# Performance work log

Measured on AMD Instinct MI355X. Metric: run time of the kernel, lower is better.

## Reference

```python
import jax, jax.numpy as jnp
import numpy as np

N = 50000      # nodes
E = 800000     # edges (avg degree 16)
H = 128        # hidden_dim
GDIM = 64      # global feature dim
G = 10         # DiffGroupNorm groups
LAMDA = 0.01
EPS = 1e-5


def setup_inputs() -> dict:
    key = jax.random.key(0)
    ks = jax.random.split(key, 24)
    s = 0.05
    inp = {
        "x": jax.random.normal(ks[0], (N, H), dtype=jnp.float32),
        "edge_index": jax.random.randint(ks[1], (2, E), 0, N, dtype=jnp.int32),
        "edge_features": jax.random.normal(ks[2], (E, H), dtype=jnp.float32),
        "global_feat": jax.random.normal(ks[3], (1, GDIM), dtype=jnp.float32),
        # combine: Dense(H) on concat [x | messages | global] -> (H+H+GDIM, H)
        "Wc": jax.random.normal(ks[4], (H + H + GDIM, H), dtype=jnp.float32) * s,
        "bc": jnp.zeros((H,), jnp.float32),
    }
    for i, tag in enumerate(["a", "b"]):
        k = jax.random.split(ks[5 + i], 4)
        inp[f"W1{tag}"] = jax.random.normal(k[0], (H, H), dtype=jnp.float32) * s
        inp[f"b1{tag}"] = jnp.zeros((H,), jnp.float32)
        inp[f"W2{tag}"] = jax.random.normal(k[1], (H, H), dtype=jnp.float32) * s
        inp[f"b2{tag}"] = jnp.zeros((H,), jnp.float32)
        inp[f"linW{tag}"] = jax.random.normal(k[2], (H, G), dtype=jnp.float32) * s
        inp[f"linb{tag}"] = jnp.zeros((G,), jnp.float32)
        inp[f"gamma{tag}"] = jnp.ones((G * H,), jnp.float32)
        inp[f"beta{tag}"] = jnp.zeros((G * H,), jnp.float32)
    return inp


def _diff_group_norm(x, linW, linb, gamma, beta):
    # DiffGroupNorm: soft group assignment + per-(group,channel) batch norm.
    n, f = x.shape
    s = jax.nn.softmax(x @ linW + linb, axis=-1)            # [N, G]
    o = (s[:, :, None] * x[:, None, :]).reshape(n, G * f)   # [N, G*F]
    mu = o.mean(axis=0)
    var = o.var(axis=0)
    o = (o - mu) * jax.lax.rsqrt(var + EPS) * gamma + beta
    return x + LAMDA * o.reshape(n, G, f).sum(axis=1)


def _block(out, W1, b1, W2, b2, linW, linb, gamma, beta):
    h = jax.nn.softplus(out @ W1 + b1) @ W2 + b2
    h = _diff_group_norm(h, linW, linb, gamma, beta)
    return out + h


def reference(x, edge_index, edge_features, global_feat, Wc, bc,
              W1a, b1a, W2a, b2a, linWa, linba, gammaa, betaa,
              W1b, b1b, W2b, b2b, linWb, linbb, gammab, betab):
    n = x.shape[0]
    row = edge_index[0]
    # tf.scatter_nd accumulates duplicates -> segment sum over destination nodes
    messages = jax.ops.segment_sum(edge_features, row, num_segments=n)
    g = jnp.repeat(global_feat, n // global_feat.shape[0], axis=0)
    combined = jnp.concatenate([x, messages, g], axis=-1)
    out = jax.nn.softplus(combined @ Wc + bc)
    initial = out
    out = _block(out, W1a, b1a, W2a, b2a, linWa, linba, gammaa, betaa)
    out = _block(out, W1b, b1b, W2b, b2b, linWb, linbb, gammab, betab)
    return out + initial
```

## Files before the change

kernel.cpp:

```cpp
#include <hip/hip_runtime.h>
#include <math.h>

constexpr int NN = 50000;
constexpr int NE = 800000;
constexpr int HD = 128;
constexpr int NG = 10;
constexpr float LAM = 0.01f;
constexpr float EPSV = 1e-5f;
constexpr int NBLK = (NN + 255) / 256;

typedef __attribute__((ext_vector_type(8))) short s8v;
typedef __attribute__((ext_vector_type(4))) float f4v;

__device__ __forceinline__ float softplus_f(float x) {
    return fmaxf(x, 0.f) + log1pf(expf(-fabsf(x)));
}
__device__ __forceinline__ unsigned short f2b(float f) {
    unsigned u = __float_as_uint(f);
    unsigned r = (u + 0x7FFFu + ((u >> 16) & 1u)) >> 16;
    return (unsigned short)r;
}
__device__ __forceinline__ float b2f(unsigned short u) {
    return __uint_as_float(((unsigned)u) << 16);
}

__global__ __launch_bounds__(256) void hist_kernel(
    const int* __restrict__ rows, int* __restrict__ cnt)
{
    int e = blockIdx.x * 256 + threadIdx.x;
    if (e < NE) atomicAdd(&cnt[rows[e]], 1);
}

__global__ __launch_bounds__(256) void scan1_kernel(
    const int* __restrict__ cnt, int* __restrict__ bsum)
{
    __shared__ int red[256];
    int t = threadIdx.x;
    int i = blockIdx.x * 256 + t;
    red[t] = (i < NN) ? cnt[i] : 0;
    __syncthreads();
    for (int d = 128; d > 0; d >>= 1) {
        if (t < d) red[t] += red[t + d];
        __syncthreads();
    }
    if (t == 0) bsum[blockIdx.x] = red[0];
}

__global__ __launch_bounds__(256) void scan2_kernel(
    const int* __restrict__ bsum, int* __restrict__ bbase)
{
    __shared__ int sh[256];
    int t = threadIdx.x;
    int v = (t < NBLK) ? bsum[t] : 0;
    sh[t] = v;
    __syncthreads();
    for (int d = 1; d < 256; d <<= 1) {
        int u = (t >= d) ? sh[t - d] : 0;
        __syncthreads();
        sh[t] += u;
        __syncthreads();
    }
    if (t < NBLK) bbase[t] = sh[t] - v;
}

__global__ __launch_bounds__(256) void scan3_kernel(
    const int* __restrict__ cnt, const int* __restrict__ bbase,
    int* __restrict__ off, int* __restrict__ cur)
{
    __shared__ int sh[256];
    int t = threadIdx.x;
    int i = blockIdx.x * 256 + t;
    int v = (i < NN) ? cnt[i] : 0;
    sh[t] = v;
    __syncthreads();
    for (int d = 1; d < 256; d <<= 1) {
        int u = (t >= d) ? sh[t - d] : 0;
        __syncthreads();
        sh[t] += u;
        __syncthreads();
    }
    int excl = sh[t] - v + bbase[blockIdx.x];
    if (i < NN) { off[i] = excl; cur[i] = excl; }
    if (i == NN - 1) off[NN] = NE;
}

__global__ __launch_bounds__(256) void fill_kernel(
    const int* __restrict__ rows, int* __restrict__ cur, int* __restrict__ eid)
{
    int e = blockIdx.x * 256 + threadIdx.x;
    if (e < NE) {
        int slot = atomicAdd(&cur[rows[e]], 1);
        eid[slot] = e;
    }
}

__global__ __launch_bounds__(256) void gather_kernel(
    const float* __restrict__ ef, const int* __restrict__ off,
    const int* __restrict__ eid, uint2* __restrict__ msgbf)
{
    int node = blockIdx.x * 4 + (threadIdx.x >> 6);
    if (node >= NN) return;
    int lane = threadIdx.x & 63;
    int half = lane >> 5, lc = lane & 31;
    int b = off[node], e = off[node + 1];
    float4 acc = make_float4(0.f, 0.f, 0.f, 0.f);
    for (int i = b + half; i < e; i += 2) {
        int ed = eid[i];
        float4 v = *reinterpret_cast<const float4*>(ef + (size_t)ed * HD + lc * 4);
        acc.x += v.x; acc.y += v.y; acc.z += v.z; acc.w += v.w;
    }
    acc.x += __shfl_xor(acc.x, 32);
    acc.y += __shfl_xor(acc.y, 32);
    acc.z += __shfl_xor(acc.z, 32);
    acc.w += __shfl_xor(acc.w, 32);
    if (half == 0) {
        uint2 pk;
        pk.x = (unsigned)f2b(acc.x) | ((unsigned)f2b(acc.y) << 16);
        pk.y = (unsigned)f2b(acc.z) | ((unsigned)f2b(acc.w) << 16);
        msgbf[(size_t)node * 32 + lc] = pk;
    }
}

__global__ __launch_bounds__(256) void prep_kernel(
    const float* __restrict__ Wc,
    const float* __restrict__ W1a, const float* __restrict__ W2a,
    const float* __restrict__ W1b, const float* __restrict__ W2b,
    short* __restrict__ wct, short* __restrict__ wts)
{
    int i = blockIdx.x * 256 + threadIdx.x;
    if (i < 40960) {
        int n = i / 320, kk = i % 320;
        wct[i] = (short)f2b(Wc[kk * 128 + n]);
    } else if (i < 40960 + 4 * 16384) {
        int j = i - 40960;
        int mat = j >> 14;
        int idx = j & 16383;
        int n = idx >> 7, kk = idx & 127;
        const float* src = (mat == 0) ? W1a : (mat == 1) ? W2a : (mat == 2) ? W1b : W2b;
        wts[j] = (short)f2b(src[kk * 128 + n]);
    }
}

__global__ __launch_bounds__(256) void combine_mfma_kernel(
    const float* __restrict__ x, const short* __restrict__ msgbf,
    const float* __restrict__ gf, const short* __restrict__ wct,
    const float* __restrict__ bc,
    unsigned short* __restrict__ outbf, unsigned short* __restrict__ initbf)
{
    __shared__ short As[64 * 72];
    __shared__ short Ws[128 * 72];
    __shared__ float bcs[128];
    const int tid = threadIdx.x;
    const int m0 = blockIdx.x * 64;
    if (tid < 128) bcs[tid] = bc[tid];
    const int lane = tid & 63;
    const int wv = tid >> 6;
    const int fr = lane & 15;
    const int fc = lane >> 4;

    f4v acc[8];
    #pragma unroll
    for (int ct = 0; ct < 8; ++ct) acc[ct] = (f4v){0.f, 0.f, 0.f, 0.f};

    const int arow = tid >> 2;
    const int aseg = (tid & 3) * 16;
    const int wcol = tid >> 1;
    const int wseg = (tid & 1) * 32;

    for (int c = 0; c < 5; ++c) {
        const int k0 = c * 64;
        {
            short tmp[16];
            int grow = m0 + arow;
            if (grow >= NN) {
                #pragma unroll
                for (int j = 0; j < 16; ++j) tmp[j] = 0;
            } else if (c < 2) {
                const float* src = x + (size_t)grow * 128 + k0 + aseg;
                #pragma unroll
                for (int q = 0; q < 4; ++q) {
                    float4 v = *reinterpret_cast<const float4*>(src + 4 * q);
                    tmp[4*q+0] = (short)f2b(v.x); tmp[4*q+1] = (short)f2b(v.y);
                    tmp[4*q+2] = (short)f2b(v.z); tmp[4*q+3] = (short)f2b(v.w);
                }
            } else if (c < 4) {
                const short* src = msgbf + (size_t)grow * 128 + (k0 - 128) + aseg;
                *(s8v*)tmp = *(const s8v*)src;
                *(s8v*)(tmp + 8) = *(const s8v*)(src + 8);
            } else {
                const float* src = gf + aseg;
                #pragma unroll
                for (int q = 0; q < 4; ++q) {
                    float4 v = *reinterpret_cast<const float4*>(src + 4 * q);
                    tmp[4*q+0] = (short)f2b(v.x); tmp[4*q+1] = (short)f2b(v.y);
                    tmp[4*q+2] = (short)f2b(v.z); tmp[4*q+3] = (short)f2b(v.w);
                }
            }
            *(s8v*)&As[arow * 72 + aseg] = *(s8v*)tmp;
            *(s8v*)&As[arow * 72 + aseg + 8] = *(s8v*)(tmp + 8);
        }
        {
            const short* src = wct + (size_t)wcol * 320 + k0 + wseg;
            #pragma unroll
            for (int j = 0; j < 4; ++j)
                *(s8v*)&Ws[wcol * 72 + wseg + 8 * j] = *(const s8v*)(src + 8 * j);
        }
        __syncthreads();
        const short* ap = As + (wv * 16 + fr) * 72 + fc * 8;
        const short* bp = Ws + fr * 72 + fc * 8;
        #pragma unroll
        for (int ks = 0; ks < 2; ++ks) {
            s8v a = *(const s8v*)(ap + ks * 32);
            #pragma unroll
            for (int ct = 0; ct < 8; ++ct) {
                s8v b = *(const s8v*)(bp + ct * 16 * 72 + ks * 32);
                acc[ct] = __builtin_amdgcn_mfma_f32_16x16x32_bf16(a, b, acc[ct], 0, 0, 0);
            }
        }
        __syncthreads();
    }
    const int rbase = m0 + wv * 16 + fc * 4;
    #pragma unroll
    for (int ct = 0; ct < 8; ++ct) {
        int col = ct * 16 + fr;
        float bv = bcs[col];
        #pragma unroll
        for (int r = 0; r < 4; ++r) {
            int row = rbase + r;
            if (row < NN) {
                unsigned short b = f2b(softplus_f(acc[ct][r] + bv));
                outbf[(size_t)row * 128 + col] = b;
                initbf[(size_t)row * 128 + col] = b;
            }
        }
    }
}

__global__ __launch_bounds__(256) void fused12_kernel(
    const unsigned short* __restrict__ outbf, const short* __restrict__ w1t,
    const short* __restrict__ w2t, const float* __restrict__ b1,
    const float* __restrict__ b2, const float* __restrict__ linW,
    const float* __restrict__ linb,
    unsigned short* __restrict__ hbf, float* __restrict__ sout)
{
    __shared__ short As[64 * 136];
    __shared__ short Ws[128 * 136];
    __shared__ short Ts[64 * 136];
    __shared__ float b1s[128], b2s[128];
    __shared__ float lws[128 * 11];
    __shared__ float lbs[10];
    const int tid = threadIdx.x;
    const int m0 = blockIdx.x * 64;
    if (tid < 128) { b1s[tid] = b1[tid]; b2s[tid] = b2[tid]; }
    for (int i = tid; i < 1280; i += 256) lws[(i / 10) * 11 + (i % 10)] = linW[i];
    if (tid < 10) lbs[tid] = linb[tid];
    const int lane = tid & 63;
    const int wv = tid >> 6;
    const int fr = lane & 15;
    const int fc = lane >> 4;

    {
        int row = tid >> 2, seg = (tid & 3) * 32;
        int grow = m0 + row;
        s8v v[4];
        if (grow < NN) {
            const short* src = (const short*)outbf + (size_t)grow * 128 + seg;
            #pragma unroll
            for (int j = 0; j < 4; ++j) v[j] = *(const s8v*)(src + 8 * j);
        } else {
            s8v z = {0,0,0,0,0,0,0,0};
            #pragma unroll
            for (int j = 0; j < 4; ++j) v[j] = z;
        }
        #pragma unroll
        for (int j = 0; j < 4; ++j) *(s8v*)&As[row * 136 + seg + 8 * j] = v[j];
    }
    {
        int col = tid >> 1, seg = (tid & 1) * 64;
        const short* src = w1t + (size_t)col * 128 + seg;
        #pragma unroll
        for (int j = 0; j < 8; ++j)
            *(s8v*)&Ws[col * 136 + seg + 8 * j] = *(const s8v*)(src + 8 * j);
    }
    __syncthreads();

    f4v acc[8];
    #pragma unroll
    for (int ct = 0; ct < 8; ++ct) acc[ct] = (f4v){0.f, 0.f, 0.f, 0.f};
    {
        const short* ap = As + (wv * 16 + fr) * 136 + fc * 8;
        const short* bp = Ws + fr * 136 + fc * 8;
        #pragma unroll
        for (int ks = 0; ks < 4; ++ks) {
            s8v a = *(const s8v*)(ap + ks * 32);
            #pragma unroll
            for (int ct = 0; ct < 8; ++ct) {
                s8v b = *(const s8v*)(bp + ct * 16 * 136 + ks * 32);
                acc[ct] = __builtin_amdgcn_mfma_f32_16x16x32_bf16(a, b, acc[ct], 0, 0, 0);
            }
        }
    }
    {
        int rb = wv * 16 + fc * 4;
        #pragma unroll
        for (int ct = 0; ct < 8; ++ct) {
            int col = ct * 16 + fr;
            float bv = b1s[col];
            #pragma unroll
            for (int r = 0; r < 4; ++r)
                Ts[(rb + r) * 136 + col] = (short)f2b(softplus_f(acc[ct][r] + bv));
        }
    }
    __syncthreads();
    {
        int col = tid >> 1, seg = (tid & 1) * 64;
        const short* src = w2t + (size_t)col * 128 + seg;
        #pragma unroll
        for (int j = 0; j < 8; ++j)
            *(s8v*)&Ws[col * 136 + seg + 8 * j] = *(const s8v*)(src + 8 * j);
    }
    __syncthreads();

    #pragma unroll
    for (int ct = 0; ct < 8; ++ct) acc[ct] = (f4v){0.f, 0.f, 0.f, 0.f};
    {
        const short* ap = Ts + (wv * 16 + fr) * 136 + fc * 8;
        const short* bp = Ws + fr * 136 + fc * 8;
        #pragma unroll
        for (int ks = 0; ks < 4; ++ks) {
            s8v a = *(const s8v*)(ap + ks * 32);
            #pragma unroll
            for (int ct = 0; ct < 8; ++ct) {
                s8v b = *(const s8v*)(bp + ct * 16 * 136 + ks * 32);
                acc[ct] = __builtin_amdgcn_mfma_f32_16x16x32_bf16(a, b, acc[ct], 0, 0, 0);
            }
        }
    }
    #pragma unroll
    for (int ct = 0; ct < 8; ++ct) {
        float bv = b2s[ct * 16 + fr];
        #pragma unroll
        for (int r = 0; r < 4; ++r) acc[ct][r] += bv;
    }
    float dot[4][10];
    #pragma unroll
    for (int r = 0; r < 4; ++r)
        #pragma unroll
        for (int g = 0; g < 10; ++g) dot[r][g] = 0.f;
    #pragma unroll
    for (int ct = 0; ct < 8; ++ct) {
        #pragma unroll
        for (int g = 0; g < 10; ++g) {
            float lwv = lws[(ct * 16 + fr) * 11 + g];
            #pragma unroll
            for (int r = 0; r < 4; ++r) dot[r][g] += acc[ct][r] * lwv;
        }
    }
    #pragma unroll
    for (int r = 0; r < 4; ++r)
        #pragma unroll
        for (int g = 0; g < 10; ++g) {
            float v = dot[r][g];
            v += __shfl_xor(v, 1);
            v += __shfl_xor(v, 2);
            v += __shfl_xor(v, 4);
            v += __shfl_xor(v, 8);
            dot[r][g] = v + lbs[g];
        }
    #pragma unroll
    for (int r = 0; r < 4; ++r) {
        float m = dot[r][0];
        #pragma unroll
        for (int g = 1; g < 10; ++g) m = fmaxf(m, dot[r][g]);
        float sum = 0.f;
        #pragma unroll
        for (int g = 0; g < 10; ++g) { dot[r][g] = expf(dot[r][g] - m); sum += dot[r][g]; }
        float inv = 1.f / sum;
        #pragma unroll
        for (int g = 0; g < 10; ++g) dot[r][g] *= inv;
    }
    const int growb = m0 + wv * 16 + fc * 4;
    #pragma unroll
    for (int ct = 0; ct < 8; ++ct) {
        int col = ct * 16 + fr;
        #pragma unroll
        for (int r = 0; r < 4; ++r) {
            int row = growb + r;
            if (row < NN) hbf[(size_t)row * 128 + col] = f2b(acc[ct][r]);
        }
    }
    if (fr < 10) {
        #pragma unroll
        for (int r = 0; r < 4; ++r) {
            int row = growb + r;
            if (row < NN) {
                float v = 0.f;
                #pragma unroll
                for (int g = 0; g < 10; ++g) v = (fr == g) ? dot[r][g] : v;
                sout[(size_t)row * 10 + fr] = v;
            }
        }
    }
}

__global__ __launch_bounds__(256) void stats_kernel(
    const unsigned short* __restrict__ hbf, const float* __restrict__ s,
    float* __restrict__ sum1, float* __restrict__ sum2)
{
    __shared__ float hs[64 * 128];
    __shared__ float ss[640];
    const int tid = threadIdx.x;
    const int c = tid & 127;
    const int g0 = (tid >> 7) * 5;
    float a1[5], a2[5];
    #pragma unroll
    for (int q = 0; q < 5; ++q) { a1[q] = 0.f; a2[q] = 0.f; }

    const int nchunks = (NN + 63) / 64;
    for (int chunk = blockIdx.x; chunk < nchunks; chunk += gridDim.x) {
        int nbase = chunk * 64;
        #pragma unroll
        for (int i = 0; i < 4; ++i) {
            int f = tid + i * 256;
            int row = f >> 4, col = (f & 15) * 8;
            int n = nbase + row;
            if (n < NN) {
                s8v raw = *(const s8v*)((const short*)hbf + (size_t)n * 128 + col);
                #pragma unroll
                for (int j = 0; j < 8; ++j)
                    hs[row * 128 + col + j] = b2f((unsigned short)raw[j]);
            } else {
                #pragma unroll
                for (int j = 0; j < 8; ++j) hs[row * 128 + col + j] = 0.f;
            }
        }
        for (int idx = tid; idx < 640; idx += 256) {
            int n = nbase + idx / 10;
            ss[idx] = (n < NN) ? s[(size_t)n * 10 + idx % 10] : 0.f;
        }
        __syncthreads();
        int nmax = min(64, NN - nbase);
        for (int n = 0; n < nmax; ++n) {
            float hv = hs[n * 128 + c];
            #pragma unroll
            for (int q = 0; q < 5; ++q) {
                float p = ss[n * 10 + g0 + q] * hv;
                a1[q] += p;
                a2[q] += p * p;
            }
        }
        __syncthreads();
    }
    #pragma unroll
    for (int q = 0; q < 5; ++q) {
        atomicAdd(&sum1[(g0 + q) * 128 + c], a1[q]);
        atomicAdd(&sum2[(g0 + q) * 128 + c], a2[q]);
    }
}

__global__ void finalize_kernel(
    const float* __restrict__ sum1, const float* __restrict__ sum2,
    const float* __restrict__ gamma, const float* __restrict__ beta,
    float* __restrict__ w, float* __restrict__ kvec)
{
    int c = threadIdx.x;
    float kacc = 0.f;
    const float invn = 1.f / (float)NN;
    for (int g = 0; g < NG; ++g) {
        int idx = g * 128 + c;
        float mu = sum1[idx] * invn;
        float var = sum2[idx] * invn - mu * mu;
        float inv = rsqrtf(var + EPSV);
        float wg = inv * gamma[idx];
        w[idx] = wg;
        kacc += beta[idx] - mu * wg;
    }
    kvec[c] = kacc;
}

template<bool LAST>
__global__ __launch_bounds__(256) void apply_kernel(
    const unsigned short* __restrict__ outbf_in,
    const unsigned short* __restrict__ hbf,
    const float* __restrict__ s, const float* __restrict__ w,
    const float* __restrict__ kvec, const unsigned short* __restrict__ initbf,
    float* __restrict__ dstf, unsigned short* __restrict__ outbf_out)
{
    __shared__ __align__(16) float ws_[1280];
    __shared__ float ks_[128];
    __shared__ float ss_[640];
    const int tid = threadIdx.x;
    const int m0 = blockIdx.x * 64;
    for (int i = tid; i < 320; i += 256)
        ((float4*)ws_)[i] = ((const float4*)w)[i];
    if (tid < 128) ks_[tid] = kvec[tid];
    for (int i = tid; i < 640; i += 256) {
        int n = m0 + i / 10;
        ss_[i] = (n < NN) ? s[(size_t)n * 10 + i % 10] : 0.f;
    }
    __syncthreads();
    const int tc = tid & 31, rg = tid >> 5;
    #pragma unroll
    for (int p = 0; p < 8; ++p) {
        int nl = p * 8 + rg;
        int n = m0 + nl;
        if (n >= NN) continue;
        float A0 = 0.f, A1 = 0.f, A2 = 0.f, A3 = 0.f;
        #pragma unroll
        for (int g = 0; g < 10; ++g) {
            float sv = ss_[nl * 10 + g];
            float4 wv = *reinterpret_cast<const float4*>(&ws_[g * 128 + tc * 4]);
            A0 += sv * wv.x; A1 += sv * wv.y; A2 += sv * wv.z; A3 += sv * wv.w;
        }
        ushort4 hv4 = *reinterpret_cast<const ushort4*>(hbf + (size_t)n * 128 + tc * 4);
        ushort4 ov4 = *reinterpret_cast<const ushort4*>(outbf_in + (size_t)n * 128 + tc * 4);
        float h0 = b2f(hv4.x), h1 = b2f(hv4.y), h2 = b2f(hv4.z), h3 = b2f(hv4.w);
        float r0 = b2f(ov4.x) + h0 + LAM * (h0 * A0 + ks_[tc * 4 + 0]);
        float r1 = b2f(ov4.y) + h1 + LAM * (h1 * A1 + ks_[tc * 4 + 1]);
        float r2 = b2f(ov4.z) + h2 + LAM * (h2 * A2 + ks_[tc * 4 + 2]);
        float r3 = b2f(ov4.w) + h3 + LAM * (h3 * A3 + ks_[tc * 4 + 3]);
        if (LAST) {
            ushort4 iv4 = *reinterpret_cast<const ushort4*>(initbf + (size_t)n * 128 + tc * 4);
            r0 += b2f(iv4.x); r1 += b2f(iv4.y); r2 += b2f(iv4.z); r3 += b2f(iv4.w);
            float4 o = make_float4(r0, r1, r2, r3);
            *reinterpret_cast<float4*>(dstf + (size_t)n * 128 + tc * 4) = o;
        } else {
            ushort4 o;
            o.x = f2b(r0); o.y = f2b(r1); o.z = f2b(r2); o.w = f2b(r3);
            *reinterpret_cast<ushort4*>(outbf_out + (size_t)n * 128 + tc * 4) = o;
        }
    }
}

extern "C" void kernel_launch(void* const* d_in, const int* in_sizes, int n_in,
                              void* d_out, int out_size, void* d_ws, size_t ws_size,
                              hipStream_t stream)
{
    const float* x    = (const float*)d_in[0];
    const int*   eidx = (const int*)  d_in[1];
    const float* ef   = (const float*)d_in[2];
    const float* gf   = (const float*)d_in[3];
    const float* Wc   = (const float*)d_in[4];
    const float* bc   = (const float*)d_in[5];

    float* p = (float*)d_ws;
    int*   cnt  = (int*)p;
    float* sums = p + NN;
    p += NN + 4 * 1280;
    unsigned short* msgbf  = (unsigned short*)p;  p += (size_t)NN * 64;
    unsigned short* outbf  = (unsigned short*)p;  p += (size_t)NN * 64;
    unsigned short* initbf = (unsigned short*)p;  p += (size_t)NN * 64;
    unsigned short* hbf    = (unsigned short*)p;  p += (size_t)NN * 64;
    float* sbuf = p;                              p += (size_t)NN * 10;
    float* wbuf = p;                              p += 1280;
    float* kvec = p;                              p += 128;
    short* wct  = (short*)p;
    short* wts  = wct + 40960;

    int* off   = (int*)initbf;
    int* cur   = off + NN + 1;
    int* bsum  = cur + NN;
    int* bbase = bsum + NBLK;
    int* eid   = (int*)hbf;

    prep_kernel<<<416, 256, 0, stream>>>(
        Wc, (const float*)d_in[6], (const float*)d_in[8],
        (const float*)d_in[14], (const float*)d_in[16], wct, wts);

    hipMemsetAsync(cnt, 0, sizeof(int) * (NN + 4 * 1280), stream);

    hist_kernel <<<(NE + 255) / 256, 256, 0, stream>>>(eidx, cnt);
    scan1_kernel<<<NBLK, 256, 0, stream>>>(cnt, bsum);
    scan2_kernel<<<1, 256, 0, stream>>>(bsum, bbase);
    scan3_kernel<<<NBLK, 256, 0, stream>>>(cnt, bbase, off, cur);
    fill_kernel <<<(NE + 255) / 256, 256, 0, stream>>>(eidx, cur, eid);
    gather_kernel<<<(NN + 3) / 4, 256, 0, stream>>>(ef, off, eid, (uint2*)msgbf);

    const int gblocks = (NN + 63) / 64;
    combine_mfma_kernel<<<gblocks, 256, 0, stream>>>(
        x, (const short*)msgbf, gf, wct, bc, outbf, initbf);

    for (int b = 0; b < 2; ++b) {
        const float* b1    = (const float*)d_in[7 + 8 * b];
        const float* b2    = (const float*)d_in[9 + 8 * b];
        const float* linW  = (const float*)d_in[10 + 8 * b];
        const float* linb  = (const float*)d_in[11 + 8 * b];
        const float* gamma = (const float*)d_in[12 + 8 * b];
        const float* beta  = (const float*)d_in[13 + 8 * b];
        const short* w1t = wts + (size_t)(2 * b) * 16384;
        const short* w2t = wts + (size_t)(2 * b + 1) * 16384;
        float* sum1 = sums + (size_t)b * 2560;
        float* sum2 = sum1 + 1280;

        fused12_kernel<<<gblocks, 256, 0, stream>>>(
            outbf, w1t, w2t, b1, b2, linW, linb, hbf, sbuf);
        stats_kernel<<<256, 256, 0, stream>>>(hbf, sbuf, sum1, sum2);
        finalize_kernel<<<1, 128, 0, stream>>>(sum1, sum2, gamma, beta, wbuf, kvec);
        if (b == 0)
            apply_kernel<false><<<gblocks, 256, 0, stream>>>(
                outbf, hbf, sbuf, wbuf, kvec, nullptr, nullptr, outbf);
        else
            apply_kernel<true><<<gblocks, 256, 0, stream>>>(
                outbf, hbf, sbuf, wbuf, kvec, initbf, (float*)d_out, nullptr);
    }
}
```

Before: 436.2 us.

## Fuse group-norm stats into GEMM kernel and drop duplicate init buffer

Per-block DiffGroupNorm partial sums are now computed inside fused12_kernel from the tile still held in LDS and written to a per-block buffer. A small deterministic reduce kernel replaces the stats kernel with global atomics, and finalize is folded into apply_kernel. The two-pass prefix scan is merged into one kernel, hist and fill are vectorised to four edges per thread, and ping-pong output buffers remove the duplicate init write. This cuts the re-read of h, the atomics and several launches, at the cost of more LDS in fused12, which may lower occupancy.

```diff
diff --git a/kernel.cpp b/kernel.cpp
--- a/kernel.cpp
+++ b/kernel.cpp
@@ -8,6 +8,7 @@
 constexpr float LAM = 0.01f;
 constexpr float EPSV = 1e-5f;
 constexpr int NBLK = (NN + 255) / 256;
+constexpr int GBLK = (NN + 63) / 64;
 
 typedef __attribute__((ext_vector_type(8))) short s8v;
 typedef __attribute__((ext_vector_type(4))) float f4v;
@@ -27,8 +28,14 @@
 __global__ __launch_bounds__(256) void hist_kernel(
     const int* __restrict__ rows, int* __restrict__ cnt)
 {
-    int e = blockIdx.x * 256 + threadIdx.x;
-    if (e < NE) atomicAdd(&cnt[rows[e]], 1);
+    int base = (blockIdx.x * 256 + threadIdx.x) * 4;
+    if (base < NE) {
+        int4 r = *reinterpret_cast<const int4*>(rows + base);
+        atomicAdd(&cnt[r.x], 1);
+        atomicAdd(&cnt[r.y], 1);
+        atomicAdd(&cnt[r.z], 1);
+        atomicAdd(&cnt[r.w], 1);
+    }
 }
 
 __global__ __launch_bounds__(256) void scan1_kernel(
@@ -46,40 +53,29 @@
     if (t == 0) bsum[blockIdx.x] = red[0];
 }
 
-__global__ __launch_bounds__(256) void scan2_kernel(
-    const int* __restrict__ bsum, int* __restrict__ bbase)
+__global__ __launch_bounds__(256) void scan3_kernel(
+    const int* __restrict__ cnt, const int* __restrict__ bsum,
+    int* __restrict__ off, int* __restrict__ cur)
 {
     __shared__ int sh[256];
-    int t = threadIdx.x;
-    int v = (t < NBLK) ? bsum[t] : 0;
-    sh[t] = v;
-    __syncthreads();
-    for (int d = 1; d < 256; d <<= 1) {
-        int u = (t >= d) ? sh[t - d] : 0;
-        __syncthreads();
-        sh[t] += u;
-        __syncthreads();
-    }
-    if (t < NBLK) bbase[t] = sh[t] - v;
-}
-
-__global__ __launch_bounds__(256) void scan3_kernel(
-    const int* __restrict__ cnt, const int* __restrict__ bbase,
-    int* __restrict__ off, int* __restrict__ cur)
-{
-    __shared__ int sh[256];
+    __shared__ int bs[256];
+    __shared__ int basev;
     int t = threadIdx.x;
     int i = blockIdx.x * 256 + t;
-    int v = (i < NN) ? cnt[i] : 0;
-    sh[t] = v;
+    int v  = (i < NN) ? cnt[i] : 0;
+    int bv = (t < NBLK) ? bsum[t] : 0;
+    sh[t] = v; bs[t] = bv;
     __syncthreads();
     for (int d = 1; d < 256; d <<= 1) {
-        int u = (t >= d) ? sh[t - d] : 0;
+        int u1 = (t >= d) ? sh[t - d] : 0;
+        int u2 = (t >= d) ? bs[t - d] : 0;
         __syncthreads();
-        sh[t] += u;
+        sh[t] += u1; bs[t] += u2;
         __syncthreads();
     }
-    int excl = sh[t] - v + bbase[blockIdx.x];
+    if (t == (int)blockIdx.x) basev = bs[t] - bv;
+    __syncthreads();
+    int excl = sh[t] - v + basev;
     if (i < NN) { off[i] = excl; cur[i] = excl; }
     if (i == NN - 1) off[NN] = NE;
 }
@@ -87,10 +83,13 @@
 __global__ __launch_bounds__(256) void fill_kernel(
     const int* __restrict__ rows, int* __restrict__ cur, int* __restrict__ eid)
 {
-    int e = blockIdx.x * 256 + threadIdx.x;
-    if (e < NE) {
-        int slot = atomicAdd(&cur[rows[e]], 1);
-        eid[slot] = e;
+    int base = (blockIdx.x * 256 + threadIdx.x) * 4;
+    if (base < NE) {
+        int4 r = *reinterpret_cast<const int4*>(rows + base);
+        eid[atomicAdd(&cur[r.x], 1)] = base + 0;
+        eid[atomicAdd(&cur[r.y], 1)] = base + 1;
+        eid[atomicAdd(&cur[r.z], 1)] = base + 2;
+        eid[atomicAdd(&cur[r.w], 1)] = base + 3;
     }
 }
 
@@ -144,8 +143,7 @@
 __global__ __launch_bounds__(256) void combine_mfma_kernel(
     const float* __restrict__ x, const short* __restrict__ msgbf,
     const float* __restrict__ gf, const short* __restrict__ wct,
-    const float* __restrict__ bc,
-    unsigned short* __restrict__ outbf, unsigned short* __restrict__ initbf)
+    const float* __restrict__ bc, unsigned short* __restrict__ out0bf)
 {
     __shared__ short As[64 * 72];
     __shared__ short Ws[128 * 72];
@@ -227,11 +225,8 @@
         #pragma unroll
         for (int r = 0; r < 4; ++r) {
             int row = rbase + r;
-            if (row < NN) {
-                unsigned short b = f2b(softplus_f(acc[ct][r] + bv));
-                outbf[(size_t)row * 128 + col] = b;
-                initbf[(size_t)row * 128 + col] = b;
-            }
+            if (row < NN)
+                out0bf[(size_t)row * 128 + col] = f2b(softplus_f(acc[ct][r] + bv));
         }
     }
 }
@@ -241,14 +236,20 @@
     const short* __restrict__ w2t, const float* __restrict__ b1,
     const float* __restrict__ b2, const float* __restrict__ linW,
     const float* __restrict__ linb,
-    unsigned short* __restrict__ hbf, float* __restrict__ sout)
-{
-    __shared__ short As[64 * 136];
-    __shared__ short Ws[128 * 136];
-    __shared__ short Ts[64 * 136];
-    __shared__ float b1s[128], b2s[128];
-    __shared__ float lws[128 * 11];
-    __shared__ float lbs[10];
+    unsigned short* __restrict__ hbf, float* __restrict__ sout,
+    float* __restrict__ pstats)
+{
+    __shared__ __align__(16) char smem[76352];
+    short* As = (short*)(smem);
+    short* Ws = (short*)(smem + 17408);
+    short* Ts = (short*)(smem + 52224);
+    float* b1s = (float*)(smem + 69632);
+    float* b2s = (float*)(smem + 70144);
+    float* lws = (float*)(smem + 70656);
+    float* lbs = (float*)(smem + 76288);
+    float* hF = (float*)(smem);
+    float* sS = (float*)(smem + 33792);
+
     const int tid = threadIdx.x;
     const int m0 = blockIdx.x * 64;
     if (tid < 128) { b1s[tid] = b1[tid]; b2s[tid] = b2[tid]; }
@@ -380,13 +381,16 @@
         for (int g = 0; g < 10; ++g) dot[r][g] *= inv;
     }
     const int growb = m0 + wv * 16 + fc * 4;
+    const int rlocb = wv * 16 + fc * 4;
+    unsigned short hq[8][4];
     #pragma unroll
     for (int ct = 0; ct < 8; ++ct) {
         int col = ct * 16 + fr;
         #pragma unroll
         for (int r = 0; r < 4; ++r) {
+            hq[ct][r] = f2b(acc[ct][r]);
             int row = growb + r;
-            if (row < NN) hbf[(size_t)row * 128 + col] = f2b(acc[ct][r]);
+            if (row < NN) hbf[(size_t)row * 128 + col] = hq[ct][r];
         }
     }
     if (fr < 10) {
@@ -401,102 +405,105 @@
             }
         }
     }
-}
-
-__global__ __launch_bounds__(256) void stats_kernel(
-    const unsigned short* __restrict__ hbf, const float* __restrict__ s,
-    float* __restrict__ sum1, float* __restrict__ sum2)
-{
-    __shared__ float hs[64 * 128];
-    __shared__ float ss[640];
-    const int tid = threadIdx.x;
-    const int c = tid & 127;
-    const int g0 = (tid >> 7) * 5;
-    float a1[5], a2[5];
-    #pragma unroll
-    for (int q = 0; q < 5; ++q) { a1[q] = 0.f; a2[q] = 0.f; }
-
-    const int nchunks = (NN + 63) / 64;
-    for (int chunk = blockIdx.x; chunk < nchunks; chunk += gridDim.x) {
-        int nbase = chunk * 64;
-        #pragma unroll
-        for (int i = 0; i < 4; ++i) {
-            int f = tid + i * 256;
-            int row = f >> 4, col = (f & 15) * 8;
-            int n = nbase + row;
-            if (n < NN) {
-                s8v raw = *(const s8v*)((const short*)hbf + (size_t)n * 128 + col);
-                #pragma unroll
-                for (int j = 0; j < 8; ++j)
-                    hs[row * 128 + col + j] = b2f((unsigned short)raw[j]);
-            } else {
-                #pragma unroll
-                for (int j = 0; j < 8; ++j) hs[row * 128 + col + j] = 0.f;
+    __syncthreads();
+    #pragma unroll
+    for (int ct = 0; ct < 8; ++ct) {
+        int col = ct * 16 + fr;
+        #pragma unroll
+        for (int r = 0; r < 4; ++r) {
+            bool valid = (growb + r) < NN;
+            hF[(rlocb + r) * 132 + col] = valid ? b2f(hq[ct][r]) : 0.f;
+        }
+    }
+    if (fr < 10) {
+        #pragma unroll
+        for (int r = 0; r < 4; ++r) {
+            bool valid = (growb + r) < NN;
+            float v = 0.f;
+            #pragma unroll
+            for (int g = 0; g < 10; ++g) v = (fr == g) ? dot[r][g] : v;
+            sS[(rlocb + r) * 10 + fr] = valid ? v : 0.f;
+        }
+    }
+    __syncthreads();
+    {
+        const int c = tid & 127;
+        const int g0 = (tid >> 7) * 5;
+        float a1[5], a2[5];
+        #pragma unroll
+        for (int q = 0; q < 5; ++q) { a1[q] = 0.f; a2[q] = 0.f; }
+        for (int n = 0; n < 64; ++n) {
+            float hv = hF[n * 132 + c];
+            #pragma unroll
+            for (int q = 0; q < 5; ++q) {
+                float pv = sS[n * 10 + g0 + q] * hv;
+                a1[q] += pv;
+                a2[q] += pv * pv;
             }
         }
-        for (int idx = tid; idx < 640; idx += 256) {
-            int n = nbase + idx / 10;
-            ss[idx] = (n < NN) ? s[(size_t)n * 10 + idx % 10] : 0.f;
-        }
-        __syncthreads();
-        int nmax = min(64, NN - nbase);
-        for (int n = 0; n < nmax; ++n) {
-            float hv = hs[n * 128 + c];
-            #pragma unroll
-            for (int q = 0; q < 5; ++q) {
-                float p = ss[n * 10 + g0 + q] * hv;
-                a1[q] += p;
-                a2[q] += p * p;
-            }
-        }
-        __syncthreads();
-    }
-    #pragma unroll
-    for (int q = 0; q < 5; ++q) {
-        atomicAdd(&sum1[(g0 + q) * 128 + c], a1[q]);
-        atomicAdd(&sum2[(g0 + q) * 128 + c], a2[q]);
-    }
-}
-
-__global__ void finalize_kernel(
-    const float* __restrict__ sum1, const float* __restrict__ sum2,
-    const float* __restrict__ gamma, const float* __restrict__ beta,
-    float* __restrict__ w, float* __restrict__ kvec)
-{
-    int c = threadIdx.x;
-    float kacc = 0.f;
-    const float invn = 1.f / (float)NN;
-    for (int g = 0; g < NG; ++g) {
-        int idx = g * 128 + c;
-        float mu = sum1[idx] * invn;
-        float var = sum2[idx] * invn - mu * mu;
-        float inv = rsqrtf(var + EPSV);
-        float wg = inv * gamma[idx];
-        w[idx] = wg;
-        kacc += beta[idx] - mu * wg;
-    }
-    kvec[c] = kacc;
+        float* dst = pstats + (size_t)blockIdx.x * 2560;
+        #pragma unroll
+        for (int q = 0; q < 5; ++q) {
+            dst[(g0 + q) * 128 + c] = a1[q];
+            dst[1280 + (g0 + q) * 128 + c] = a2[q];
+        }
+    }
+}
+
+__global__ __launch_bounds__(256) void reduce_stats_kernel(
+    const float* __restrict__ pstats, float* __restrict__ sums)
+{
+    int e = blockIdx.x * 256 + threadIdx.x;
+    if (e >= 2560) return;
+    float s0 = 0.f, s1 = 0.f, s2 = 0.f, s3 = 0.f;
+    int j = 0;
+    for (; j + 3 < GBLK; j += 4) {
+        s0 += pstats[(size_t)(j + 0) * 2560 + e];
+        s1 += pstats[(size_t)(j + 1) * 2560 + e];
+        s2 += pstats[(size_t)(j + 2) * 2560 + e];
+        s3 += pstats[(size_t)(j + 3) * 2560 + e];
+    }
+    for (; j < GBLK; ++j) s0 += pstats[(size_t)j * 2560 + e];
+    sums[e] = (s0 + s1) + (s2 + s3);
 }
 
 template<bool LAST>
 __global__ __launch_bounds__(256) void apply_kernel(
     const unsigned short* __restrict__ outbf_in,
     const unsigned short* __restrict__ hbf,
-    const float* __restrict__ s, const float* __restrict__ w,
-    const float* __restrict__ kvec, const unsigned short* __restrict__ initbf,
+    const float* __restrict__ s, const float* __restrict__ sums,
+    const float* __restrict__ gamma, const float* __restrict__ beta,
+    const unsigned short* __restrict__ out0bf,
     float* __restrict__ dstf, unsigned short* __restrict__ outbf_out)
 {
     __shared__ __align__(16) float ws_[1280];
+    __shared__ float mus_[1280];
     __shared__ float ks_[128];
     __shared__ float ss_[640];
     const int tid = threadIdx.x;
     const int m0 = blockIdx.x * 64;
-    for (int i = tid; i < 320; i += 256)
-        ((float4*)ws_)[i] = ((const float4*)w)[i];
-    if (tid < 128) ks_[tid] = kvec[tid];
+    const float invn = 1.f / (float)NN;
+    for (int idx = tid; idx < 1280; idx += 256) {
+        float s1 = sums[idx], s2 = sums[idx + 1280];
+        float mu = s1 * invn;
+        float var = s2 * invn - mu * mu;
+        float wg = rsqrtf(var + EPSV) * gamma[idx];
+        ws_[idx] = wg;
+        mus_[idx] = mu;
+    }
     for (int i = tid; i < 640; i += 256) {
         int n = m0 + i / 10;
         ss_[i] = (n < NN) ? s[(size_t)n * 10 + i % 10] : 0.f;
+    }
+    __syncthreads();
+    if (tid < 128) {
+        float kacc = 0.f;
+        #pragma unroll
+        for (int g = 0; g < NG; ++g) {
+            int idx = g * 128 + tid;
+            kacc += beta[idx] - mus_[idx] * ws_[idx];
+        }
+        ks_[tid] = kacc;
     }
     __syncthreads();
     const int tc = tid & 31, rg = tid >> 5;
@@ -520,7 +527,7 @@
         float r2 = b2f(ov4.z) + h2 + LAM * (h2 * A2 + ks_[tc * 4 + 2]);
         float r3 = b2f(ov4.w) + h3 + LAM * (h3 * A3 + ks_[tc * 4 + 3]);
         if (LAST) {
-            ushort4 iv4 = *reinterpret_cast<const ushort4*>(initbf + (size_t)n * 128 + tc * 4);
+            ushort4 iv4 = *reinterpret_cast<const ushort4*>(out0bf + (size_t)n * 128 + tc * 4);
             r0 += b2f(iv4.x); r1 += b2f(iv4.y); r2 += b2f(iv4.z); r3 += b2f(iv4.w);
             float4 o = make_float4(r0, r1, r2, r3);
             *reinterpret_cast<float4*>(dstf + (size_t)n * 128 + tc * 4) = o;
@@ -544,41 +551,37 @@
     const float* bc   = (const float*)d_in[5];
 
     float* p = (float*)d_ws;
-    int*   cnt  = (int*)p;
-    float* sums = p + NN;
-    p += NN + 4 * 1280;
+    int*   cnt  = (int*)p;                        p += NN;
+    float* sums = p;                              p += 2560;
+    float* pstats = p;                            p += (size_t)GBLK * 2560;
     unsigned short* msgbf  = (unsigned short*)p;  p += (size_t)NN * 64;
-    unsigned short* outbf  = (unsigned short*)p;  p += (size_t)NN * 64;
-    unsigned short* initbf = (unsigned short*)p;  p += (size_t)NN * 64;
+    unsigned short* out0bf = (unsigned short*)p;  p += (size_t)NN * 64;
+    unsigned short* out1bf = (unsigned short*)p;  p += (size_t)NN * 64;
     unsigned short* hbf    = (unsigned short*)p;  p += (size_t)NN * 64;
     float* sbuf = p;                              p += (size_t)NN * 10;
-    float* wbuf = p;                              p += 1280;
-    float* kvec = p;                              p += 128;
     short* wct  = (short*)p;
     short* wts  = wct + 40960;
 
-    int* off   = (int*)initbf;
+    int* off   = (int*)out1bf;
     int* cur   = off + NN + 1;
     int* bsum  = cur + NN;
-    int* bbase = bsum + NBLK;
     int* eid   = (int*)hbf;
 
     prep_kernel<<<416, 256, 0, stream>>>(
         Wc, (const float*)d_in[6], (const float*)d_in[8],
         (const float*)d_in[14], (const float*)d_in[16], wct, wts);
 
-    hipMemsetAsync(cnt, 0, sizeof(int) * (NN + 4 * 1280), stream);
-
-    hist_kernel <<<(NE + 255) / 256, 256, 0, stream>>>(eidx, cnt);
+    hipMemsetAsync(cnt, 0, sizeof(int) * NN, stream);
+
+    const int eblocks = (NE / 4 + 255) / 256;
+    hist_kernel <<<eblocks, 256, 0, stream>>>(eidx, cnt);
     scan1_kernel<<<NBLK, 256, 0, stream>>>(cnt, bsum);
-    scan2_kernel<<<1, 256, 0, stream>>>(bsum, bbase);
-    scan3_kernel<<<NBLK, 256, 0, stream>>>(cnt, bbase, off, cur);
-    fill_kernel <<<(NE + 255) / 256, 256, 0, stream>>>(eidx, cur, eid);
+    scan3_kernel<<<NBLK, 256, 0, stream>>>(cnt, bsum, off, cur);
+    fill_kernel <<<eblocks, 256, 0, stream>>>(eidx, cur, eid);
     gather_kernel<<<(NN + 3) / 4, 256, 0, stream>>>(ef, off, eid, (uint2*)msgbf);
 
-    const int gblocks = (NN + 63) / 64;
-    combine_mfma_kernel<<<gblocks, 256, 0, stream>>>(
-        x, (const short*)msgbf, gf, wct, bc, outbf, initbf);
+    combine_mfma_kernel<<<GBLK, 256, 0, stream>>>(
+        x, (const short*)msgbf, gf, wct, bc, out0bf);
 
     for (int b = 0; b < 2; ++b) {
         const float* b1    = (const float*)d_in[7 + 8 * b];
@@ -589,18 +592,16 @@
         const float* beta  = (const float*)d_in[13 + 8 * b];
         const short* w1t = wts + (size_t)(2 * b) * 16384;
         const short* w2t = wts + (size_t)(2 * b + 1) * 16384;
-        float* sum1 = sums + (size_t)b * 2560;
-        float* sum2 = sum1 + 1280;
-
-        fused12_kernel<<<gblocks, 256, 0, stream>>>(
-            outbf, w1t, w2t, b1, b2, linW, linb, hbf, sbuf);
-        stats_kernel<<<256, 256, 0, stream>>>(hbf, sbuf, sum1, sum2);
-        finalize_kernel<<<1, 128, 0, stream>>>(sum1, sum2, gamma, beta, wbuf, kvec);
+        const unsigned short* outin = (b == 0) ? out0bf : out1bf;
+
+        fused12_kernel<<<GBLK, 256, 0, stream>>>(
+            outin, w1t, w2t, b1, b2, linW, linb, hbf, sbuf, pstats);
+        reduce_stats_kernel<<<10, 256, 0, stream>>>(pstats, sums);
         if (b == 0)
-            apply_kernel<false><<<gblocks, 256, 0, stream>>>(
-                outbf, hbf, sbuf, wbuf, kvec, nullptr, nullptr, outbf);
+            apply_kernel<false><<<GBLK, 256, 0, stream>>>(
+                out0bf, hbf, sbuf, sums, gamma, beta, nullptr, nullptr, out1bf);
         else
-            apply_kernel<true><<<gblocks, 256, 0, stream>>>(
-                outbf, hbf, sbuf, wbuf, kvec, initbf, (float*)d_out, nullptr);
-    }
-}
+            apply_kernel<true><<<GBLK, 256, 0, stream>>>(
+                out1bf, hbf, sbuf, sums, gamma, beta, out0bf, (float*)d_out, nullptr);
+    }
+}
```

Measured after the change: 518.1 us. 1.19x slower.
